# Kernel optimization log

Measured on AMD Instinct MI355X. Metric: run time of the kernel, lower is better.

Reference implementation:

```python
import jax, jax.numpy as jnp
import numpy as np

N_NODES = 100000
N_EDGES = 800000
F_IN = 58


def setup_inputs() -> dict:
    key = jax.random.key(0)
    ks = jax.random.split(key, 8)
    x = jax.random.normal(ks[0], (N_NODES, F_IN), dtype=jnp.float32)
    edge_index = jax.random.randint(ks[1], (2, N_EDGES), 0, N_NODES, dtype=jnp.int64)

    def glorot(k, shape):
        fan_in = shape[-2]
        return jax.random.normal(k, shape, dtype=jnp.float32) * (1.0 / np.sqrt(fan_in))

    W1 = glorot(ks[2], (2, 58, 300))
    b1 = jnp.zeros((300,), jnp.float32)
    W2 = glorot(ks[3], (2, 300, 100))
    b2 = jnp.zeros((100,), jnp.float32)
    W3 = glorot(ks[4], (2, 100, 1))
    b3 = jnp.zeros((1,), jnp.float32)
    return {"x": x, "edge_index": edge_index, "W1": W1, "b1": b1,
            "W2": W2, "b2": b2, "W3": W3, "b3": b3}


def cheb_conv_k2(x, edge_index, W, b):
    """PyG ChebConv, K=2, sym normalization, lambda_max=2:
    L_hat = -D^{-1/2} A D^{-1/2}; out = x @ W[0] + (L_hat x) @ W[1] + b."""
    src, dst = edge_index[0], edge_index[1]
    n = x.shape[0]
    ones = jnp.ones(src.shape, x.dtype)
    deg = jax.ops.segment_sum(ones, src, num_segments=n)  # degree from row index
    dinv = jnp.where(deg > 0, 1.0 / jnp.sqrt(jnp.where(deg > 0, deg, 1.0)), 0.0)
    w = -(dinv[src] * dinv[dst])                          # [E] edge weights of L_hat
    tx1 = jax.ops.segment_sum(w[:, None] * x[src], dst, num_segments=n)  # [N,F]
    return x @ W[0] + tx1 @ W[1] + b


def reference(x, edge_index, W1, b1, W2, b2, W3, b3):
    # eval mode: dropout layers are identity
    h = jax.nn.relu(cheb_conv_k2(x, edge_index, W1, b1))
    h = jax.nn.relu(cheb_conv_k2(h, edge_index, W2, b2))
    return cheb_conv_k2(h, edge_index, W3, b3)
```

## Files before the change

### kernel.cpp

```cpp
#include <hip/hip_runtime.h>


typedef short bf16x8 __attribute__((ext_vector_type(8)));
typedef float f32x4 __attribute__((ext_vector_type(4)));

__device__ __forceinline__ unsigned f2bf(float f) {
  unsigned u = __float_as_uint(f);
  u += 0x7fff + ((u >> 16) & 1);
  return u >> 16;
}
__device__ __forceinline__ float bf2f(unsigned s) {
  return __uint_as_float(s << 16);
}

__global__ void k_count_prep(
    const int* __restrict__ src, const int* __restrict__ dst,
    unsigned* __restrict__ deg, unsigned* __restrict__ cnt,
    unsigned* __restrict__ rank, int E, int EB,
    const float* __restrict__ x, unsigned short* __restrict__ xb, int N, int XB,
    const float* __restrict__ W1, uint4* __restrict__ W1f,
    const float* __restrict__ W2, uint4* __restrict__ W2f,
    const float* __restrict__ b1, float* __restrict__ b1pad) {
  int b = blockIdx.x, t = threadIdx.x;
  if (b < EB) {
    int i = b * 256 + t;
    if (i < E) {
      atomicAdd(&deg[src[i]], 1u);
      rank[i] = atomicAdd(&cnt[dst[i]], 1u);
    }
    return;
  }
  b -= EB;
  if (b < XB) {
    int idx = b * 256 + t;
    int n = idx >> 6, p = idx & 63;
    if (n >= N) return;
    int c = p * 2;
    if (c < 58) {
      unsigned lo = f2bf(x[(size_t)n * 58 + c]);
      unsigned hi = f2bf(x[(size_t)n * 58 + c + 1]);
      *(unsigned*)(xb + (size_t)n * 128 + c) = lo | (hi << 16);
    } else if (c >= 116) {
      *(unsigned*)(xb + (size_t)n * 128 + c) = 0;
    }
    return;
  }
  b -= XB;
  if (b < 20) {
    int idx = b * 256 + t;
    int lane = idx & 63, j = (idx >> 6) % 20, s = (idx >> 6) / 20;
    int lr = lane & 15, g = lane >> 4;
    int c = j * 16 + lr;
    unsigned short v[8];
#pragma unroll
    for (int i = 0; i < 8; i++) {
      int k = s * 32 + g * 8 + i;
      float f = 0.0f;
      if (c < 300 && k < 116)
        f = (k < 58) ? W1[k * 300 + c] : W1[17400 + (k - 58) * 300 + c];
      v[i] = (unsigned short)f2bf(f);
    }
    W1f[idx] = *(const uint4*)v;
    return;
  }
  b -= 20;
  if (b < 33) {
    int idx = b * 256 + t;
    if (idx >= 10 * 13 * 64) return;
    int lane = idx & 63, j = (idx >> 6) % 13, s = (idx >> 6) / 13;
    int lr = lane & 15, g = lane >> 4;
    int r = j * 16 + lr;
    unsigned short v[8];
#pragma unroll
    for (int i = 0; i < 8; i++) {
      int k = s * 32 + g * 8 + i;
      float f = 0.0f;
      if (k < 300) {
        if (r < 100) f = W2[30000 + k * 100 + r];
        else if (r >= 104 && r < 204) f = W2[k * 100 + (r - 104)];
      }
      v[i] = (unsigned short)f2bf(f);
    }
    W2f[idx] = *(const uint4*)v;
    return;
  }
  b -= 33;
  {
    int idx = b * 256 + t;
    if (idx < 320) b1pad[idx] = (idx < 300) ? b1[idx] : 0.0f;
  }
}

__global__ void k_dinv(const unsigned* __restrict__ deg, float* __restrict__ dinv, int N) {
  int i = blockIdx.x * blockDim.x + threadIdx.x;
  if (i < N) {
    unsigned d = deg[i];
    dinv[i] = d ? rsqrtf((float)d) : 0.0f;
  }
}

__global__ __launch_bounds__(256) void k_scan1(const unsigned* __restrict__ cnt,
                                               unsigned* __restrict__ btot, int N) {
  __shared__ unsigned s[256];
  int b = blockIdx.x, t = threadIdx.x;
  int base = b * 1024;
  unsigned sum = 0;
  for (int i = t; i < 1024; i += 256) {
    int idx = base + i;
    sum += (idx < N) ? cnt[idx] : 0u;
  }
  s[t] = sum;
  __syncthreads();
  for (int off = 128; off > 0; off >>= 1) {
    if (t < off) s[t] += s[t + off];
    __syncthreads();
  }
  if (t == 0) btot[b] = s[0];
}

__global__ __launch_bounds__(256) void k_scan2(unsigned* __restrict__ btot,
                                               unsigned* __restrict__ rowstart,
                                               int NB, int N, int E) {
  __shared__ unsigned s[256];
  int t = threadIdx.x;
  s[t] = (t < NB) ? btot[t] : 0u;
  __syncthreads();
  if (t == 0) {
    unsigned acc = 0;
    for (int i = 0; i < NB; i++) { unsigned v = s[i]; s[i] = acc; acc += v; }
  }
  __syncthreads();
  if (t < NB) btot[t] = s[t];
  if (t == 0) rowstart[N] = (unsigned)E;
}

__global__ __launch_bounds__(256) void k_scan3(const unsigned* __restrict__ cnt,
                                               const unsigned* __restrict__ btot,
                                               unsigned* __restrict__ rowstart, int N) {
  __shared__ unsigned ssum[256];
  int b = blockIdx.x, t = threadIdx.x;
  int base = b * 1024 + t * 4;
  unsigned v0 = 0, v1 = 0, v2 = 0, v3 = 0;
  if (base + 0 < N) v0 = cnt[base + 0];
  if (base + 1 < N) v1 = cnt[base + 1];
  if (base + 2 < N) v2 = cnt[base + 2];
  if (base + 3 < N) v3 = cnt[base + 3];
  ssum[t] = v0 + v1 + v2 + v3;
  __syncthreads();
  for (int off = 1; off < 256; off <<= 1) {
    unsigned add = (t >= off) ? ssum[t - off] : 0u;
    __syncthreads();
    ssum[t] += add;
    __syncthreads();
  }
  unsigned texcl = ((t == 0) ? 0u : ssum[t - 1]) + btot[b];
  unsigned r0 = texcl, r1 = r0 + v0, r2 = r1 + v1, r3 = r2 + v2;
  if (base + 0 < N) rowstart[base + 0] = r0;
  if (base + 1 < N) rowstart[base + 1] = r1;
  if (base + 2 < N) rowstart[base + 2] = r2;
  if (base + 3 < N) rowstart[base + 3] = r3;
}

__global__ void k_fill(const int* __restrict__ src, const int* __restrict__ dst,
                       const float* __restrict__ dinv, const unsigned* __restrict__ rowstart,
                       const unsigned* __restrict__ rank, int2* __restrict__ er, int E) {
  int e = blockIdx.x * blockDim.x + threadIdx.x;
  if (e >= E) return;
  int s = src[e], d = dst[e];
  er[rowstart[d] + rank[e]] = make_int2(s, __float_as_int(dinv[s]));
}

__global__ __launch_bounds__(256) void k_gather58(
    const unsigned* __restrict__ rowstart, const int2* __restrict__ er,
    const float* __restrict__ dinv, unsigned short* __restrict__ xb, int N) {
  int pair = (blockIdx.x * blockDim.x + threadIdx.x) >> 6;
  int lane = threadIdx.x & 63;
  int wid = pair * 2 + (lane >> 5);
  int c0 = (lane & 31) * 2;
  if (wid >= N || c0 >= 58) return;
  unsigned s0 = rowstart[wid], s1 = rowstart[wid + 1];
  float a0[8], a1[8];
#pragma unroll
  for (int k = 0; k < 8; k++) { a0[k] = 0.f; a1[k] = 0.f; }
  for (unsigned e = s0; e < s1; e += 8) {
    int2 r[8];
#pragma unroll
    for (int k = 0; k < 8; k++) {
      unsigned idx = e + k;
      r[k] = er[idx < s1 ? idx : s1 - 1];
    }
    unsigned v[8];
#pragma unroll
    for (int k = 0; k < 8; k++)
      v[k] = *(const unsigned*)(xb + (size_t)r[k].x * 128 + c0);
#pragma unroll
    for (int k = 0; k < 8; k++) {
      float w = (e + k < s1) ? __int_as_float(r[k].y) : 0.f;
      a0[k] += w * bf2f(v[k] & 0xffffu);
      a1[k] += w * bf2f(v[k] >> 16);
    }
  }
  float dd = -dinv[wid];
  float p0 = dd * (((a0[0] + a0[1]) + (a0[2] + a0[3])) + ((a0[4] + a0[5]) + (a0[6] + a0[7])));
  float p1 = dd * (((a1[0] + a1[1]) + (a1[2] + a1[3])) + ((a1[4] + a1[5]) + (a1[6] + a1[7])));
  *(unsigned*)(xb + (size_t)wid * 128 + 58 + c0) = f2bf(p0) | (f2bf(p1) << 16);
}

__global__ __launch_bounds__(256) void k_gather_l2(
    const unsigned* __restrict__ rowstart, const int2* __restrict__ er,
    const float* __restrict__ dinv, const unsigned short* __restrict__ ga2b,
    const float* __restrict__ b2, const float* __restrict__ W30,
    const float* __restrict__ W31, const float* __restrict__ b3,
    float* __restrict__ a3, float* __restrict__ g3, int N) {
  int wid = (blockIdx.x * blockDim.x + threadIdx.x) >> 6;
  if (wid >= N) return;
  int lane = threadIdx.x & 63;
  int c0 = lane * 2;
  bool act = c0 < 100;
  unsigned s0 = rowstart[wid], s1 = rowstart[wid + 1];
  float aa = 0.f, gg = 0.f;
  if (act) {
    float a0[8], a1[8];
#pragma unroll
    for (int k = 0; k < 8; k++) { a0[k] = 0.f; a1[k] = 0.f; }
    for (unsigned e = s0; e < s1; e += 8) {
      int2 r[8];
#pragma unroll
      for (int k = 0; k < 8; k++) {
        unsigned idx = e + k;
        r[k] = er[idx < s1 ? idx : s1 - 1];
      }
      unsigned v[8];
#pragma unroll
      for (int k = 0; k < 8; k++)
        v[k] = *(const unsigned*)(ga2b + (size_t)r[k].x * 208 + c0);
#pragma unroll
      for (int k = 0; k < 8; k++) {
        float w = (e + k < s1) ? __int_as_float(r[k].y) : 0.f;
        a0[k] += w * bf2f(v[k] & 0xffffu);
        a1[k] += w * bf2f(v[k] >> 16);
      }
    }
    float dd = -dinv[wid];
    float p0 = dd * (((a0[0] + a0[1]) + (a0[2] + a0[3])) + ((a0[4] + a0[5]) + (a0[6] + a0[7])));
    float p1 = dd * (((a1[0] + a1[1]) + (a1[2] + a1[3])) + ((a1[4] + a1[5]) + (a1[6] + a1[7])));
    unsigned av = *(const unsigned*)(ga2b + (size_t)wid * 208 + 104 + c0);
    float h0 = fmaxf(bf2f(av & 0xffffu) + p0 + b2[c0], 0.f);
    float h1 = fmaxf(bf2f(av >> 16) + p1 + b2[c0 + 1], 0.f);
    aa = h0 * W30[c0] + h1 * W30[c0 + 1];
    gg = h0 * W31[c0] + h1 * W31[c0 + 1];
  }
#pragma unroll
  for (int off = 32; off > 0; off >>= 1) {
    aa += __shfl_xor(aa, off);
    gg += __shfl_xor(gg, off);
  }
  if (lane == 0) {
    a3[wid] = aa + b3[0];
    g3[wid] = gg;
  }
}

__global__ void k_gather1(const unsigned* __restrict__ rowstart, const int2* __restrict__ er,
                          const float* __restrict__ dinv, const float* __restrict__ g3,
                          const float* __restrict__ a3, float* __restrict__ out, int N) {
  int n = blockIdx.x * blockDim.x + threadIdx.x;
  if (n >= N) return;
  unsigned s0 = rowstart[n], s1 = rowstart[n + 1];
  float a[8];
#pragma unroll
  for (int k = 0; k < 8; k++) a[k] = 0.f;
  for (unsigned e = s0; e < s1; e += 8) {
    int2 r[8];
#pragma unroll
    for (int k = 0; k < 8; k++) {
      unsigned idx = e + k;
      r[k] = er[idx < s1 ? idx : s1 - 1];
    }
    float gv[8];
#pragma unroll
    for (int k = 0; k < 8; k++) gv[k] = g3[r[k].x];
#pragma unroll
    for (int k = 0; k < 8; k++) {
      float w = (e + k < s1) ? __int_as_float(r[k].y) : 0.f;
      a[k] += w * gv[k];
    }
  }
  float sum = ((a[0] + a[1]) + (a[2] + a[3])) + ((a[4] + a[5]) + (a[6] + a[7]));
  out[n] = a3[n] - dinv[n] * sum;
}

#define STG 324
__global__ __launch_bounds__(256, 3) void k_mm12_mfma(
    const unsigned short* __restrict__ xb, const uint4* __restrict__ W1f,
    const uint4* __restrict__ W2f, const float* __restrict__ b1pad,
    unsigned short* __restrict__ ga2b) {
  __shared__ unsigned short stage[4 * 16 * STG];
  int tid = threadIdx.x;
  int lane = tid & 63, wv = tid >> 6, lr = lane & 15, g = lane >> 4;
  int n0 = blockIdx.x * 64 + wv * 16;
  unsigned short* ost = stage + wv * 16 * STG;

  bf16x8 a1[4];
#pragma unroll
  for (int s = 0; s < 4; s++)
    a1[s] = *(const bf16x8*)(xb + (size_t)(n0 + lr) * 128 + s * 32 + g * 8);
#pragma unroll
  for (int half = 0; half < 2; half++) {
    f32x4 acc[10];
#pragma unroll
    for (int j = 0; j < 10; j++) acc[j] = (f32x4){0.f, 0.f, 0.f, 0.f};
#pragma unroll
    for (int s = 0; s < 4; s++) {
      bf16x8 w[10];
#pragma unroll
      for (int j = 0; j < 10; j++)
        w[j] = *(const bf16x8*)&W1f[(s * 20 + half * 10 + j) * 64 + lane];
      __builtin_amdgcn_sched_barrier(0);
#pragma unroll
      for (int j = 0; j < 10; j++)
        acc[j] = __builtin_amdgcn_mfma_f32_16x16x32_bf16(w[j], a1[s], acc[j], 0, 0, 0);
    }
#pragma unroll
    for (int j = 0; j < 10; j++) {
      int c = half * 160 + j * 16 + g * 4;
      float4 bv = *(const float4*)(b1pad + c);
      unsigned lo = f2bf(fmaxf(acc[j][0] + bv.x, 0.f)) |
                    (f2bf(fmaxf(acc[j][1] + bv.y, 0.f)) << 16);
      unsigned hi = f2bf(fmaxf(acc[j][2] + bv.z, 0.f)) |
                    (f2bf(fmaxf(acc[j][3] + bv.w, 0.f)) << 16);
      uint2 pk; pk.x = lo; pk.y = hi;
      *(uint2*)(ost + lr * STG + c) = pk;
    }
  }

  uint2 pk0[7], pk1[6];
  {
    f32x4 acc[7];
#pragma unroll
    for (int j = 0; j < 7; j++) acc[j] = (f32x4){0.f, 0.f, 0.f, 0.f};
#pragma unroll
    for (int s = 0; s < 10; s++) {
      bf16x8 a = *(const bf16x8*)(ost + lr * STG + s * 32 + g * 8);
      bf16x8 w[7];
#pragma unroll
      for (int j = 0; j < 7; j++) w[j] = *(const bf16x8*)&W2f[(s * 13 + j) * 64 + lane];
      __builtin_amdgcn_sched_barrier(0);
#pragma unroll
      for (int j = 0; j < 7; j++)
        acc[j] = __builtin_amdgcn_mfma_f32_16x16x32_bf16(w[j], a, acc[j], 0, 0, 0);
    }
#pragma unroll
    for (int j = 0; j < 7; j++) {
      pk0[j].x = f2bf(acc[j][0]) | (f2bf(acc[j][1]) << 16);
      pk0[j].y = f2bf(acc[j][2]) | (f2bf(acc[j][3]) << 16);
    }
  }
  {
    f32x4 acc[6];
#pragma unroll
    for (int j = 0; j < 6; j++) acc[j] = (f32x4){0.f, 0.f, 0.f, 0.f};
#pragma unroll
    for (int s = 0; s < 10; s++) {
      bf16x8 a = *(const bf16x8*)(ost + lr * STG + s * 32 + g * 8);
      bf16x8 w[6];
#pragma unroll
      for (int j = 0; j < 6; j++) w[j] = *(const bf16x8*)&W2f[(s * 13 + 7 + j) * 64 + lane];
      __builtin_amdgcn_sched_barrier(0);
#pragma unroll
      for (int j = 0; j < 6; j++)
        acc[j] = __builtin_amdgcn_mfma_f32_16x16x32_bf16(w[j], a, acc[j], 0, 0, 0);
    }
#pragma unroll
    for (int j = 0; j < 6; j++) {
      pk1[j].x = f2bf(acc[j][0]) | (f2bf(acc[j][1]) << 16);
      pk1[j].y = f2bf(acc[j][2]) | (f2bf(acc[j][3]) << 16);
    }
  }
#pragma unroll
  for (int j = 0; j < 7; j++)
    *(uint2*)(ost + lr * 216 + j * 16 + g * 4) = pk0[j];
#pragma unroll
  for (int j = 0; j < 6; j++)
    *(uint2*)(ost + lr * 216 + (7 + j) * 16 + g * 4) = pk1[j];
  uint4* gdst = (uint4*)(ga2b + (size_t)n0 * 208);
  for (int idx = lane; idx < 416; idx += 64) {
    int row = idx / 26, q = idx - row * 26;
    gdst[idx] = *(const uint4*)(ost + row * 216 + q * 8);
  }
}

extern "C" void kernel_launch(void* const* d_in, const int* in_sizes, int n_in,
                              void* d_out, int out_size, void* d_ws, size_t ws_size,
                              hipStream_t stream) {
  const float* x  = (const float*)d_in[0];
  const int*   ei = (const int*)d_in[1];
  const float* W1 = (const float*)d_in[2];
  const float* b1 = (const float*)d_in[3];
  const float* W2 = (const float*)d_in[4];
  const float* b2 = (const float*)d_in[5];
  const float* W3 = (const float*)d_in[6];
  const float* b3 = (const float*)d_in[7];
  float* out = (float*)d_out;

  const int N = in_sizes[0] / 58;
  const int E = in_sizes[1] / 2;
  const int NR = (N + 127) & ~127;
  const int NB = (N + 1023) / 1024;
  const int* src = ei;
  const int* dst = ei + E;

  char* ws = (char*)d_ws;
  size_t off = 0;
  auto alloc = [&](size_t bytes) -> void* {
    void* p = ws + off;
    off += (bytes + 255) & ~(size_t)255;
    return p;
  };
  unsigned* deg      = (unsigned*)alloc((size_t)2 * N * 4);
  unsigned* cnt      = deg + N;
  float*    dinv     = (float*)alloc((size_t)N * 4);
  unsigned* rowstart = (unsigned*)alloc((size_t)(N + 1) * 4);
  unsigned* rank     = (unsigned*)alloc((size_t)E * 4);
  unsigned* btot     = (unsigned*)alloc((size_t)256 * 4);
  int2*     er       = (int2*)alloc((size_t)E * 8);
  unsigned short* xb   = (unsigned short*)alloc((size_t)NR * 128 * 2);
  uint4*    W1f      = (uint4*)alloc((size_t)4 * 20 * 64 * 16);
  uint4*    W2f      = (uint4*)alloc((size_t)10 * 13 * 64 * 16);
  float*    b1pad    = (float*)alloc((size_t)320 * 4);
  unsigned short* ga2b = (unsigned short*)alloc((size_t)NR * 208 * 2);
  float* a3 = (float*)alloc((size_t)N * 4);
  float* g3 = (float*)alloc((size_t)N * 4);

  const int EB = (E + 255) / 256;
  const int XB = ((size_t)N * 64 + 255) / 256;

  hipMemsetAsync(deg, 0, (size_t)2 * N * 4, stream);
  k_count_prep<<<EB + XB + 20 + 33 + 2, 256, 0, stream>>>(
      src, dst, deg, cnt, rank, E, EB, x, xb, N, XB, W1, W1f, W2, W2f, b1, b1pad);
  k_dinv<<<(N + 255) / 256, 256, 0, stream>>>(deg, dinv, N);
  k_scan1<<<NB, 256, 0, stream>>>(cnt, btot, N);
  k_scan2<<<1, 256, 0, stream>>>(btot, rowstart, NB, N, E);
  k_scan3<<<NB, 256, 0, stream>>>(cnt, btot, rowstart, N);
  k_fill<<<(E + 255) / 256, 256, 0, stream>>>(src, dst, dinv, rowstart, rank, er, E);

  k_gather58<<<((N + 1) / 2 * 64 + 255) / 256, 256, 0, stream>>>(rowstart, er, dinv, xb, N);
  k_mm12_mfma<<<NR / 64, 256, 0, stream>>>(xb, W1f, W2f, b1pad, ga2b);
  k_gather_l2<<<(N + 3) / 4, 256, 0, stream>>>(rowstart, er, dinv, ga2b,
                                               b2, W3, W3 + 100, b3, a3, g3, N);

  k_gather1<<<(N + 255) / 256, 256, 0, stream>>>(rowstart, er, dinv, g3, a3, out, N);
}
```

Baseline: 271.0 us.

## Process two 16-row tiles per wave in fused MFMA matmul kernel

Each wave now computes 32 node rows (two 16-row MFMA tiles) instead of 16, so every weight fragment loaded from global memory feeds two MFMAs. The block shrinks to 128 threads (2 waves) covering the same 64 rows, with launch bounds changed to 128 threads and 2 blocks per CU. This halves weight-load traffic per output row, at the cost of doubled accumulator registers per wave (40 f32x4 in layer 1) and likely lower occupancy.

```diff
diff --git a/kernel.cpp b/kernel.cpp
--- a/kernel.cpp
+++ b/kernel.cpp
@@ -291,25 +291,29 @@
 }
 
 #define STG 324
-__global__ __launch_bounds__(256, 3) void k_mm12_mfma(
+__global__ __launch_bounds__(128, 2) void k_mm12_mfma(
     const unsigned short* __restrict__ xb, const uint4* __restrict__ W1f,
     const uint4* __restrict__ W2f, const float* __restrict__ b1pad,
     unsigned short* __restrict__ ga2b) {
-  __shared__ unsigned short stage[4 * 16 * STG];
+  __shared__ unsigned short stage[2 * 32 * STG];
   int tid = threadIdx.x;
   int lane = tid & 63, wv = tid >> 6, lr = lane & 15, g = lane >> 4;
-  int n0 = blockIdx.x * 64 + wv * 16;
-  unsigned short* ost = stage + wv * 16 * STG;
-
-  bf16x8 a1[4];
-#pragma unroll
-  for (int s = 0; s < 4; s++)
-    a1[s] = *(const bf16x8*)(xb + (size_t)(n0 + lr) * 128 + s * 32 + g * 8);
+  int n0 = blockIdx.x * 64 + wv * 32;
+  unsigned short* ost = stage + wv * 32 * STG;
+
+  bf16x8 a1[2][4];
+#pragma unroll
+  for (int t = 0; t < 2; t++)
+#pragma unroll
+    for (int s = 0; s < 4; s++)
+      a1[t][s] = *(const bf16x8*)(xb + (size_t)(n0 + t * 16 + lr) * 128 + s * 32 + g * 8);
 #pragma unroll
   for (int half = 0; half < 2; half++) {
-    f32x4 acc[10];
-#pragma unroll
-    for (int j = 0; j < 10; j++) acc[j] = (f32x4){0.f, 0.f, 0.f, 0.f};
+    f32x4 acc[2][10];
+#pragma unroll
+    for (int t = 0; t < 2; t++)
+#pragma unroll
+      for (int j = 0; j < 10; j++) acc[t][j] = (f32x4){0.f, 0.f, 0.f, 0.f};
 #pragma unroll
     for (int s = 0; s < 4; s++) {
       bf16x8 w[10];
@@ -318,73 +322,94 @@
         w[j] = *(const bf16x8*)&W1f[(s * 20 + half * 10 + j) * 64 + lane];
       __builtin_amdgcn_sched_barrier(0);
 #pragma unroll
-      for (int j = 0; j < 10; j++)
-        acc[j] = __builtin_amdgcn_mfma_f32_16x16x32_bf16(w[j], a1[s], acc[j], 0, 0, 0);
-    }
-#pragma unroll
-    for (int j = 0; j < 10; j++) {
-      int c = half * 160 + j * 16 + g * 4;
-      float4 bv = *(const float4*)(b1pad + c);
-      unsigned lo = f2bf(fmaxf(acc[j][0] + bv.x, 0.f)) |
-                    (f2bf(fmaxf(acc[j][1] + bv.y, 0.f)) << 16);
-      unsigned hi = f2bf(fmaxf(acc[j][2] + bv.z, 0.f)) |
-                    (f2bf(fmaxf(acc[j][3] + bv.w, 0.f)) << 16);
-      uint2 pk; pk.x = lo; pk.y = hi;
-      *(uint2*)(ost + lr * STG + c) = pk;
-    }
-  }
-
-  uint2 pk0[7], pk1[6];
+      for (int j = 0; j < 10; j++) {
+        acc[0][j] = __builtin_amdgcn_mfma_f32_16x16x32_bf16(w[j], a1[0][s], acc[0][j], 0, 0, 0);
+        acc[1][j] = __builtin_amdgcn_mfma_f32_16x16x32_bf16(w[j], a1[1][s], acc[1][j], 0, 0, 0);
+      }
+    }
+#pragma unroll
+    for (int t = 0; t < 2; t++)
+#pragma unroll
+      for (int j = 0; j < 10; j++) {
+        int c = half * 160 + j * 16 + g * 4;
+        float4 bv = *(const float4*)(b1pad + c);
+        unsigned lo = f2bf(fmaxf(acc[t][j][0] + bv.x, 0.f)) |
+                      (f2bf(fmaxf(acc[t][j][1] + bv.y, 0.f)) << 16);
+        unsigned hi = f2bf(fmaxf(acc[t][j][2] + bv.z, 0.f)) |
+                      (f2bf(fmaxf(acc[t][j][3] + bv.w, 0.f)) << 16);
+        uint2 pk; pk.x = lo; pk.y = hi;
+        *(uint2*)(ost + (t * 16 + lr) * STG + c) = pk;
+      }
+  }
+
+  uint2 pk0[2][7], pk1[2][6];
   {
-    f32x4 acc[7];
-#pragma unroll
-    for (int j = 0; j < 7; j++) acc[j] = (f32x4){0.f, 0.f, 0.f, 0.f};
+    f32x4 acc[2][7];
+#pragma unroll
+    for (int t = 0; t < 2; t++)
+#pragma unroll
+      for (int j = 0; j < 7; j++) acc[t][j] = (f32x4){0.f, 0.f, 0.f, 0.f};
 #pragma unroll
     for (int s = 0; s < 10; s++) {
-      bf16x8 a = *(const bf16x8*)(ost + lr * STG + s * 32 + g * 8);
+      bf16x8 a0 = *(const bf16x8*)(ost + lr * STG + s * 32 + g * 8);
+      bf16x8 a1v = *(const bf16x8*)(ost + (16 + lr) * STG + s * 32 + g * 8);
       bf16x8 w[7];
 #pragma unroll
       for (int j = 0; j < 7; j++) w[j] = *(const bf16x8*)&W2f[(s * 13 + j) * 64 + lane];
       __builtin_amdgcn_sched_barrier(0);
 #pragma unroll
-      for (int j = 0; j < 7; j++)
-        acc[j] = __builtin_amdgcn_mfma_f32_16x16x32_bf16(w[j], a, acc[j], 0, 0, 0);
-    }
-#pragma unroll
-    for (int j = 0; j < 7; j++) {
-      pk0[j].x = f2bf(acc[j][0]) | (f2bf(acc[j][1]) << 16);
-      pk0[j].y = f2bf(acc[j][2]) | (f2bf(acc[j][3]) << 16);
-    }
+      for (int j = 0; j < 7; j++) {
+        acc[0][j] = __builtin_amdgcn_mfma_f32_16x16x32_bf16(w[j], a0, acc[0][j], 0, 0, 0);
+        acc[1][j] = __builtin_amdgcn_mfma_f32_16x16x32_bf16(w[j], a1v, acc[1][j], 0, 0, 0);
+      }
+    }
+#pragma unroll
+    for (int t = 0; t < 2; t++)
+#pragma unroll
+      for (int j = 0; j < 7; j++) {
+        pk0[t][j].x = f2bf(acc[t][j][0]) | (f2bf(acc[t][j][1]) << 16);
+        pk0[t][j].y = f2bf(acc[t][j][2]) | (f2bf(acc[t][j][3]) << 16);
+      }
   }
   {
-    f32x4 acc[6];
-#pragma unroll
-    for (int j = 0; j < 6; j++) acc[j] = (f32x4){0.f, 0.f, 0.f, 0.f};
+    f32x4 acc[2][6];
+#pragma unroll
+    for (int t = 0; t < 2; t++)
+#pragma unroll
+      for (int j = 0; j < 6; j++) acc[t][j] = (f32x4){0.f, 0.f, 0.f, 0.f};
 #pragma unroll
     for (int s = 0; s < 10; s++) {
-      bf16x8 a = *(const bf16x8*)(ost + lr * STG + s * 32 + g * 8);
+      bf16x8 a0 = *(const bf16x8*)(ost + lr * STG + s * 32 + g * 8);
+      bf16x8 a1v = *(const bf16x8*)(ost + (16 + lr) * STG + s * 32 + g * 8);
       bf16x8 w[6];
 #pragma unroll
       for (int j = 0; j < 6; j++) w[j] = *(const bf16x8*)&W2f[(s * 13 + 7 + j) * 64 + lane];
       __builtin_amdgcn_sched_barrier(0);
 #pragma unroll
-      for (int j = 0; j < 6; j++)
-        acc[j] = __builtin_amdgcn_mfma_f32_16x16x32_bf16(w[j], a, acc[j], 0, 0, 0);
-    }
-#pragma unroll
-    for (int j = 0; j < 6; j++) {
-      pk1[j].x = f2bf(acc[j][0]) | (f2bf(acc[j][1]) << 16);
-      pk1[j].y = f2bf(acc[j][2]) | (f2bf(acc[j][3]) << 16);
-    }
-  }
-#pragma unroll
-  for (int j = 0; j < 7; j++)
-    *(uint2*)(ost + lr * 216 + j * 16 + g * 4) = pk0[j];
-#pragma unroll
-  for (int j = 0; j < 6; j++)
-    *(uint2*)(ost + lr * 216 + (7 + j) * 16 + g * 4) = pk1[j];
+      for (int j = 0; j < 6; j++) {
+        acc[0][j] = __builtin_amdgcn_mfma_f32_16x16x32_bf16(w[j], a0, acc[0][j], 0, 0, 0);
+        acc[1][j] = __builtin_amdgcn_mfma_f32_16x16x32_bf16(w[j], a1v, acc[1][j], 0, 0, 0);
+      }
+    }
+#pragma unroll
+    for (int t = 0; t < 2; t++)
+#pragma unroll
+      for (int j = 0; j < 6; j++) {
+        pk1[t][j].x = f2bf(acc[t][j][0]) | (f2bf(acc[t][j][1]) << 16);
+        pk1[t][j].y = f2bf(acc[t][j][2]) | (f2bf(acc[t][j][3]) << 16);
+      }
+  }
+#pragma unroll
+  for (int t = 0; t < 2; t++) {
+#pragma unroll
+    for (int j = 0; j < 7; j++)
+      *(uint2*)(ost + (t * 16 + lr) * 216 + j * 16 + g * 4) = pk0[t][j];
+#pragma unroll
+    for (int j = 0; j < 6; j++)
+      *(uint2*)(ost + (t * 16 + lr) * 216 + (7 + j) * 16 + g * 4) = pk1[t][j];
+  }
   uint4* gdst = (uint4*)(ga2b + (size_t)n0 * 208);
-  for (int idx = lane; idx < 416; idx += 64) {
+  for (int idx = lane; idx < 832; idx += 64) {
     int row = idx / 26, q = idx - row * 26;
     gdst[idx] = *(const uint4*)(ost + row * 216 + q * 8);
   }
@@ -445,7 +470,7 @@
   k_fill<<<(E + 255) / 256, 256, 0, stream>>>(src, dst, dinv, rowstart, rank, er, E);
 
   k_gather58<<<((N + 1) / 2 * 64 + 255) / 256, 256, 0, stream>>>(rowstart, er, dinv, xb, N);
-  k_mm12_mfma<<<NR / 64, 256, 0, stream>>>(xb, W1f, W2f, b1pad, ga2b);
+  k_mm12_mfma<<<NR / 64, 128, 0, stream>>>(xb, W1f, W2f, b1pad, ga2b);
   k_gather_l2<<<(N + 3) / 4, 256, 0, stream>>>(rowstart, er, dinv, ga2b,
                                                b2, W3, W3 + 100, b3, a3, g3, N);
 
```

New measurement: 265.6 us. 2.0% less time.
